# Optimization experiments

Hardware: AMD Instinct MI355X
Metric: run time of the kernel (lower is better)

## Reference

```python
import jax, jax.numpy as jnp
import numpy as np

N, E, R, D = 50000, 800000, 8, 64
BN_EPS = 1e-5


def _bn_relu(x, g, b):
    # training-mode BatchNorm1d (biased variance) + relu
    m = x.mean(axis=0)
    v = x.var(axis=0)
    return jax.nn.relu((x - m) / jnp.sqrt(v + BN_EPS) * g + b)


def setup_inputs() -> dict:
    key = jax.random.key(0)
    ks = jax.random.split(key, 10)
    return {
        'x': jax.random.normal(ks[0], (N, D), dtype=jnp.float32),
        'edge_weight': jax.random.uniform(ks[1], (E,), dtype=jnp.float32),
        'W_lin1': jax.random.normal(ks[2], (D, R * D), dtype=jnp.float32) * 0.05,
        'b_lin1': jnp.zeros((D,), jnp.float32),
        'W_self1': jax.random.normal(ks[3], (D, D), dtype=jnp.float32) * 0.05,
        'b_self1': jnp.zeros((D,), jnp.float32),
        'gamma1': jnp.ones((D,), jnp.float32),
        'beta1': jnp.zeros((D,), jnp.float32),
        'W_lin2': jax.random.normal(ks[4], (D, D), dtype=jnp.float32) * 0.05,
        'b_lin2': jnp.zeros((D,), jnp.float32),
        'W_self2': jax.random.normal(ks[5], (D, D), dtype=jnp.float32) * 0.05,
        'b_self2': jnp.zeros((D,), jnp.float32),
        'gamma2': jnp.ones((D,), jnp.float32),
        'beta2': jnp.zeros((D,), jnp.float32),
        'node_in': jax.random.randint(ks[6], (E,), 0, N, dtype=jnp.int32),
        'node_out': jax.random.randint(ks[7], (E,), 0, N, dtype=jnp.int32),
        'relation': jax.random.randint(ks[8], (E,), 0, R, dtype=jnp.int32),
        'num_relation': R,
    }


def reference(x, edge_weight, W_lin1, b_lin1, W_self1, b_self1, gamma1, beta1,
              W_lin2, b_lin2, W_self2, b_self2, gamma2, beta2,
              node_in, node_out, relation, num_relation):
    Nn, Din = x.shape
    Rr = int(num_relation)
    seg = node_out * Rr + relation  # node_out * num_relation + relation
    # degree normalization of edge weights (shared by both layers)
    deg = jax.ops.segment_sum(edge_weight, seg, num_segments=Nn * Rr)
    ew = edge_weight / deg[seg]

    # layer 1: relationalGraphConv
    msgs = x[node_in] * ew[:, None]  # [E, D]
    upd = jax.ops.segment_sum(msgs, seg, num_segments=Nn * Rr)
    upd = upd.reshape(Nn, Rr * Din)  # node-major flatten, matches torch .view
    h = upd @ W_lin1.T + b_lin1 + x @ W_self1.T + b_self1
    h = _bn_relu(h, gamma1, beta1)  # [N, D]

    # layer 2: relationalGraph (per-relation outputs)
    msgs2 = h[node_in] * ew[:, None]
    upd2 = jax.ops.segment_sum(msgs2, seg, num_segments=Nn * Rr)  # [N*R, D] node-major
    upd2 = upd2.reshape(Nn, Rr, -1).transpose(1, 0, 2).reshape(Rr * Nn, -1)  # relation-major
    h_rep = jnp.tile(h, (Rr, 1))  # input.repeat(R, 1)
    out = upd2 @ W_lin2.T + b_lin2 + h_rep @ W_self2.T + b_self2
    out = _bn_relu(out, gamma2, beta2)
    return out.reshape(Rr, Nn, -1)
```

## Files before the change

kernel.cpp:

```cpp
#include <hip/hip_runtime.h>


#define GATHER_GRID 2048
#define SCAN_CHUNK 4096
#define RED_BLOCKS 64
#define ZERO_BLOCKS 256
#define PACK_BLOCKS 16
#define XB_BLOCKS 64
#define COUNT_BLOCKS 2048
#define PLACE_BLOCKS 1024
#define STAT1_BLOCKS 512

typedef short bf16x8 __attribute__((ext_vector_type(8)));
typedef float f32x4 __attribute__((ext_vector_type(4)));

static __device__ __forceinline__ float bf2f(unsigned short u) {
  return __uint_as_float(((unsigned)u) << 16);
}
static __device__ __forceinline__ unsigned short f2bf(float f) {
  unsigned u = __float_as_uint(f);
  u += 0x7FFFu + ((u >> 16) & 1u);
  return (unsigned short)(u >> 16);
}

__global__ void k_zeropack(int* __restrict__ cnt, int NR, int R,
                           const float* __restrict__ Wlin1, const float* __restrict__ Wself1,
                           const float* __restrict__ Wlin2, const float* __restrict__ Wself2,
                           unsigned short* __restrict__ wb1, unsigned short* __restrict__ wb2) {
  if (blockIdx.x < ZERO_BLOCKS) {
    int i = blockIdx.x * 256 + threadIdx.x;
    int stride = ZERO_BLOCKS * 256;
    for (int k = i; k < NR; k += stride) cnt[k] = 0;
  } else {
    int i = (blockIdx.x - ZERO_BLOCKS) * 256 + threadIdx.x;
    int stride = PACK_BLOCKS * 256;
    int KW = R * 64 + 64;
    int n1 = 64 * KW;
    int n2 = 2 * 64 * 64;
    for (int t = i; t < n1 + n2; t += stride) {
      if (t < n1) {
        int j = t / KW, k = t - j * KW;
        float v = (k < R * 64) ? Wlin1[j * (R * 64) + k] : Wself1[j * 64 + (k - R * 64)];
        wb1[t] = f2bf(v);
      } else {
        int t2 = t - n1;
        int r = t2 >> 6, d = t2 & 63;
        float v = (r < 64) ? Wlin2[r * 64 + d] : Wself2[(r - 64) * 64 + d];
        wb2[t2] = f2bf(v);
      }
    }
  }
}

__global__ void k_countx(const int* __restrict__ node_out, const int* __restrict__ rel,
                         int* __restrict__ cnt, int* __restrict__ tmp, int E, int R,
                         const float4* __restrict__ xin, ushort4* __restrict__ xb, int n4) {
  if (blockIdx.x < XB_BLOCKS) {
    int i = blockIdx.x * 256 + threadIdx.x;
    int stride = XB_BLOCKS * 256;
    for (int k = i; k < n4; k += stride) {
      float4 v = xin[k];
      ushort4 o;
      o.x = f2bf(v.x); o.y = f2bf(v.y); o.z = f2bf(v.z); o.w = f2bf(v.w);
      xb[k] = o;
    }
  } else {
    int i = (blockIdx.x - XB_BLOCKS) * 256 + threadIdx.x;
    int stride = COUNT_BLOCKS * 256;
    for (int e = i; e < E; e += stride) {
      int seg = node_out[e] * R + rel[e];
      tmp[e] = atomicAdd(&cnt[seg], 1);
    }
  }
}

__global__ __launch_bounds__(256) void k_scan1(const int* __restrict__ cnt,
                                               int* __restrict__ bsum, int NR) {
  __shared__ int red[256];
  int tid = threadIdx.x;
  int base = blockIdx.x * SCAN_CHUNK;
  int s = 0;
  for (int i = tid; i < SCAN_CHUNK; i += 256) {
    int idx = base + i;
    if (idx < NR) s += cnt[idx];
  }
  red[tid] = s;
  __syncthreads();
  for (int off = 128; off > 0; off >>= 1) {
    if (tid < off) red[tid] += red[tid + off];
    __syncthreads();
  }
  if (tid == 0) bsum[blockIdx.x] = red[0];
}

__global__ void k_scan2(const int* __restrict__ bsum, int* __restrict__ bpre,
                        int* __restrict__ rowptr_end, int NB) {
  int lane = threadIdx.x;
  int carry = 0;
  for (int base = 0; base < NB; base += 64) {
    int i = base + lane;
    int v = (i < NB) ? bsum[i] : 0;
    int incl = v;
    #pragma unroll
    for (int off = 1; off < 64; off <<= 1) {
      int u = __shfl_up(incl, off);
      if (lane >= off) incl += u;
    }
    if (i < NB) bpre[i] = carry + incl - v;
    carry += __shfl(incl, 63);
  }
  if (lane == 0) *rowptr_end = carry;
}

__global__ __launch_bounds__(256) void k_scan3(const int* __restrict__ cnt,
                                               const int* __restrict__ bpre,
                                               int* __restrict__ rowptr, int NR) {
  __shared__ int wtot[4];
  int tid = threadIdx.x, lane = tid & 63, wid = tid >> 6;
  int base = blockIdx.x * SCAN_CHUNK + tid * 16;
  int v[16];
  int t = 0;
  #pragma unroll
  for (int i = 0; i < 16; i++) {
    int idx = base + i;
    v[i] = (idx < NR) ? cnt[idx] : 0;
    t += v[i];
  }
  int incl = t;
  #pragma unroll
  for (int off = 1; off < 64; off <<= 1) {
    int u = __shfl_up(incl, off);
    if (lane >= off) incl += u;
  }
  if (lane == 63) wtot[wid] = incl;
  __syncthreads();
  int woff = 0;
  for (int w = 0; w < wid; w++) woff += wtot[w];
  int start = bpre[blockIdx.x] + woff + incl - t;
  #pragma unroll
  for (int i = 0; i < 16; i++) {
    int idx = base + i;
    if (idx < NR) rowptr[idx] = start;
    start += v[i];
  }
}

__global__ void k_place(const float* __restrict__ w, const int* __restrict__ node_out,
                        const int* __restrict__ node_in, const int* __restrict__ rel,
                        const int* __restrict__ rowptr, const int* __restrict__ tmp,
                        unsigned* __restrict__ ep4, int E, int R) {
  int i = blockIdx.x * blockDim.x + threadIdx.x;
  int stride = gridDim.x * blockDim.x;
  for (int e = i; e < E; e += stride) {
    int seg = node_out[e] * R + rel[e];
    int pos = rowptr[seg] + tmp[e];
    ep4[pos] = (unsigned)node_in[e] | ((unsigned)f2bf(w[e]) << 16);
  }
}

__global__ void k_norm(const int* __restrict__ rowptr, unsigned* __restrict__ ep4, int NR) {
  int s = blockIdx.x * blockDim.x + threadIdx.x;
  if (s >= NR) return;
  int k0 = rowptr[s], k1 = rowptr[s + 1];
  if (k0 >= k1) return;
  float d = 0.f;
  for (int k = k0; k < k1; k++) d += bf2f((unsigned short)(ep4[k] >> 16));
  float inv = 1.f / d;
  for (int k = k0; k < k1; k++) {
    unsigned v = ep4[k];
    float w = bf2f((unsigned short)(v >> 16)) * inv;
    ep4[k] = (v & 0xFFFFu) | ((unsigned)f2bf(w) << 16);
  }
}

__global__ __launch_bounds__(256) void k_gatherx(
    const int* __restrict__ rowptr, const unsigned* __restrict__ ep4,
    const unsigned short* __restrict__ xb, unsigned short* __restrict__ updx,
    int N, int R) {
  int lane = threadIdx.x & 63;
  int wid = threadIdx.x >> 6;
  int l16 = lane & 15;
  int lg = lane >> 4;
  int c0 = l16 * 4;
  int grp = blockIdx.x * 16 + wid * 4 + lg;
  int ngrp = gridDim.x * 16;
  for (int n = grp; n < N; n += ngrp) {
    int segbase = n * R;
    int k = rowptr[segbase];
    for (int r = 0; r < R; r++) {
      int k1 = rowptr[segbase + r + 1];
      float a0 = 0.f, a1 = 0.f, a2 = 0.f, a3 = 0.f;
      for (; k + 1 < k1; k += 2) {
        unsigned pA = ep4[k], pB = ep4[k + 1];
        ushort4 uA = *(const ushort4*)&xb[(size_t)(pA & 0xFFFFu) * 64 + c0];
        ushort4 uB = *(const ushort4*)&xb[(size_t)(pB & 0xFFFFu) * 64 + c0];
        float wA = bf2f((unsigned short)(pA >> 16));
        float wB = bf2f((unsigned short)(pB >> 16));
        a0 = fmaf(wA, bf2f(uA.x), a0); a1 = fmaf(wA, bf2f(uA.y), a1);
        a2 = fmaf(wA, bf2f(uA.z), a2); a3 = fmaf(wA, bf2f(uA.w), a3);
        a0 = fmaf(wB, bf2f(uB.x), a0); a1 = fmaf(wB, bf2f(uB.y), a1);
        a2 = fmaf(wB, bf2f(uB.z), a2); a3 = fmaf(wB, bf2f(uB.w), a3);
      }
      if (k < k1) {
        unsigned p = ep4[k];
        float w = bf2f((unsigned short)(p >> 16));
        ushort4 u = *(const ushort4*)&xb[(size_t)(p & 0xFFFFu) * 64 + c0];
        a0 = fmaf(w, bf2f(u.x), a0); a1 = fmaf(w, bf2f(u.y), a1);
        a2 = fmaf(w, bf2f(u.z), a2); a3 = fmaf(w, bf2f(u.w), a3);
        k = k1;
      }
      ushort4 o; o.x = f2bf(a0); o.y = f2bf(a1); o.z = f2bf(a2); o.w = f2bf(a3);
      *(ushort4*)&updx[(size_t)n * 512 + r * 64 + c0] = o;
    }
  }
}

__global__ __launch_bounds__(256) void k_gemm1b(
    const unsigned short* __restrict__ updx, const unsigned short* __restrict__ xb,
    int M, const unsigned short* __restrict__ wb1, unsigned short* __restrict__ h_pre) {
  int m0 = blockIdx.x * 64;
  int wid = threadIdx.x >> 6;
  int lane = threadIdx.x & 63;
  int mrow = m0 + wid * 16 + (lane & 15);
  int mload = (mrow < M) ? mrow : (M - 1);
  int koff = 8 * (lane >> 4);
  const unsigned short* aU = updx + (size_t)mload * 512 + koff;
  const unsigned short* aX = xb + (size_t)mload * 64 + koff;
  const unsigned short* wr = wb1 + (size_t)(lane & 15) * 576 + koff;
  f32x4 acc[4] = {{0,0,0,0},{0,0,0,0},{0,0,0,0},{0,0,0,0}};
  #pragma unroll
  for (int kk = 0; kk < 16; ++kk) {
    bf16x8 a = *(const bf16x8*)(aU + kk * 32);
    #pragma unroll
    for (int nt = 0; nt < 4; ++nt) {
      bf16x8 b = *(const bf16x8*)(wr + (size_t)nt * 16 * 576 + kk * 32);
      acc[nt] = __builtin_amdgcn_mfma_f32_16x16x32_bf16(a, b, acc[nt], 0, 0, 0);
    }
  }
  #pragma unroll
  for (int kk = 0; kk < 2; ++kk) {
    bf16x8 a = *(const bf16x8*)(aX + kk * 32);
    #pragma unroll
    for (int nt = 0; nt < 4; ++nt) {
      bf16x8 b = *(const bf16x8*)(wr + (size_t)nt * 16 * 576 + 512 + kk * 32);
      acc[nt] = __builtin_amdgcn_mfma_f32_16x16x32_bf16(a, b, acc[nt], 0, 0, 0);
    }
  }
  int rbase = m0 + wid * 16 + ((lane >> 4) << 2);
  int cbase = lane & 15;
  #pragma unroll
  for (int nt = 0; nt < 4; ++nt) {
    int col = nt * 16 + cbase;
    #pragma unroll
    for (int rg = 0; rg < 4; ++rg) {
      int grow = rbase + rg;
      if (grow < M) h_pre[(size_t)grow * 64 + col] = f2bf(acc[nt][rg]);
    }
  }
}

__global__ __launch_bounds__(256) void k_stats1(const unsigned short* __restrict__ h,
                                                int N, float* __restrict__ part) {
  int j = threadIdx.x & 63;
  int rg = threadIdx.x >> 6;
  float s = 0.f, q = 0.f;
  for (int row = blockIdx.x * 4 + rg; row < N; row += gridDim.x * 4) {
    float v = bf2f(h[(size_t)row * 64 + j]);
    s += v; q += v * v;
  }
  __shared__ float sp[4][64], sq[4][64];
  sp[rg][j] = s; sq[rg][j] = q;
  __syncthreads();
  if (threadIdx.x < 64) {
    float ss = 0.f, qq = 0.f;
    for (int g = 0; g < 4; g++) { ss += sp[g][threadIdx.x]; qq += sq[g][threadIdx.x]; }
    part[(size_t)blockIdx.x * 128 + threadIdx.x] = ss;
    part[(size_t)blockIdx.x * 128 + 64 + threadIdx.x] = qq;
  }
}

__global__ __launch_bounds__(256) void k_gemm2bn(
    const unsigned short* __restrict__ hp, int M,
    const unsigned short* __restrict__ Wb, int nslab,
    const float* __restrict__ ss,
    unsigned short* __restrict__ outLinB, unsigned short* __restrict__ outSelf) {
  __shared__ float sss[128];
  if (threadIdx.x < 128) sss[threadIdx.x] = ss[threadIdx.x];
  __syncthreads();
  int m0 = blockIdx.x * 64;
  int wid = threadIdx.x >> 6;
  int lane = threadIdx.x & 63;
  int mrow = m0 + wid * 16 + (lane & 15);
  int mload = (mrow < M) ? mrow : (M - 1);
  int cb = 8 * (lane >> 4);
  const unsigned short* arow = hp + (size_t)mload * 64 + cb;
  ushort4 u0 = *(const ushort4*)(arow);
  ushort4 u1 = *(const ushort4*)(arow + 4);
  ushort4 u2 = *(const ushort4*)(arow + 32);
  ushort4 u3 = *(const ushort4*)(arow + 36);
  bf16x8 a0, a1;
  #pragma unroll
  for (int j = 0; j < 4; j++) {
    unsigned short uu0 = (&u0.x)[j], uu1 = (&u1.x)[j], uu2 = (&u2.x)[j], uu3 = (&u3.x)[j];
    a0[j]     = (short)f2bf(fmaxf(fmaf(bf2f(uu0), sss[cb + j],      sss[64 + cb + j]), 0.f));
    a0[j + 4] = (short)f2bf(fmaxf(fmaf(bf2f(uu1), sss[cb + 4 + j],  sss[64 + cb + 4 + j]), 0.f));
    a1[j]     = (short)f2bf(fmaxf(fmaf(bf2f(uu2), sss[cb + 32 + j], sss[64 + cb + 32 + j]), 0.f));
    a1[j + 4] = (short)f2bf(fmaxf(fmaf(bf2f(uu3), sss[cb + 36 + j], sss[64 + cb + 36 + j]), 0.f));
  }
  int rbase = m0 + wid * 16 + ((lane >> 4) << 2);
  int cbase = lane & 15;
  for (int slab = 0; slab <= nslab; ++slab) {
    const unsigned short* wrow = Wb + ((size_t)slab * 64 + (lane & 15)) * 64 + 8 * (lane >> 4);
    unsigned short* op = (slab < nslab) ? (outLinB + (size_t)slab * M * 64) : outSelf;
    #pragma unroll
    for (int nt = 0; nt < 4; ++nt) {
      bf16x8 b0 = *(const bf16x8*)(wrow + nt * 16 * 64);
      bf16x8 b1 = *(const bf16x8*)(wrow + nt * 16 * 64 + 32);
      f32x4 c = {};
      c = __builtin_amdgcn_mfma_f32_16x16x32_bf16(a0, b0, c, 0, 0, 0);
      c = __builtin_amdgcn_mfma_f32_16x16x32_bf16(a1, b1, c, 0, 0, 0);
      int col = nt * 16 + cbase;
      #pragma unroll
      for (int rg = 0; rg < 4; ++rg) {
        int grow = rbase + rg;
        if (grow < M) op[(size_t)grow * 64 + col] = f2bf(c[rg]);
      }
    }
  }
}

__global__ __launch_bounds__(256) void k_gather2_stats(
    const int* __restrict__ rowptr, const unsigned* __restrict__ ep4,
    const unsigned short* __restrict__ z, const unsigned short* __restrict__ s2,
    float* __restrict__ part, int N, int R) {
  int lane = threadIdx.x & 63;
  int wid = threadIdx.x >> 6;
  int l16 = lane & 15;
  int lg = lane >> 4;
  int c0 = l16 * 4;
  int grp = blockIdx.x * 16 + wid * 4 + lg;
  int ngrp = gridDim.x * 16;
  int NR = N * R;
  float lsum[4] = {0.f, 0.f, 0.f, 0.f}, lsq[4] = {0.f, 0.f, 0.f, 0.f};
  for (int s = grp; s < NR; s += ngrp) {
    unsigned r = (unsigned)s / (unsigned)N;
    int n = s - (int)r * N;
    int seg = n * R + (int)r;
    int k = rowptr[seg];
    int k1 = rowptr[seg + 1];
    float a0 = 0.f, a1 = 0.f, a2 = 0.f, a3 = 0.f;
    for (; k + 1 < k1; k += 2) {
      unsigned pA = ep4[k], pB = ep4[k + 1];
      ushort4 uA = *(const ushort4*)&z[(size_t)(pA & 0xFFFFu) * 64 + c0];
      ushort4 uB = *(const ushort4*)&z[(size_t)(pB & 0xFFFFu) * 64 + c0];
      float wA = bf2f((unsigned short)(pA >> 16));
      float wB = bf2f((unsigned short)(pB >> 16));
      a0 = fmaf(wA, bf2f(uA.x), a0); a1 = fmaf(wA, bf2f(uA.y), a1);
      a2 = fmaf(wA, bf2f(uA.z), a2); a3 = fmaf(wA, bf2f(uA.w), a3);
      a0 = fmaf(wB, bf2f(uB.x), a0); a1 = fmaf(wB, bf2f(uB.y), a1);
      a2 = fmaf(wB, bf2f(uB.z), a2); a3 = fmaf(wB, bf2f(uB.w), a3);
    }
    if (k < k1) {
      unsigned p = ep4[k];
      float w = bf2f((unsigned short)(p >> 16));
      ushort4 u = *(const ushort4*)&z[(size_t)(p & 0xFFFFu) * 64 + c0];
      a0 = fmaf(w, bf2f(u.x), a0); a1 = fmaf(w, bf2f(u.y), a1);
      a2 = fmaf(w, bf2f(u.z), a2); a3 = fmaf(w, bf2f(u.w), a3);
    }
    ushort4 su = *(const ushort4*)&s2[(size_t)n * 64 + c0];
    float v0 = a0 + bf2f(su.x), v1 = a1 + bf2f(su.y);
    float v2 = a2 + bf2f(su.z), v3 = a3 + bf2f(su.w);
    lsum[0] += v0; lsq[0] += v0 * v0;
    lsum[1] += v1; lsq[1] += v1 * v1;
    lsum[2] += v2; lsq[2] += v2 * v2;
    lsum[3] += v3; lsq[3] += v3 * v3;
  }
  __shared__ float sp[16][64], sq[16][64];
  int g = wid * 4 + lg;
  #pragma unroll
  for (int i = 0; i < 4; i++) { sp[g][c0 + i] = lsum[i]; sq[g][c0 + i] = lsq[i]; }
  __syncthreads();
  if (threadIdx.x < 64) {
    int j = threadIdx.x;
    float s = 0.f, q = 0.f;
    #pragma unroll
    for (int gg = 0; gg < 16; gg++) { s += sp[gg][j]; q += sq[gg][j]; }
    part[(size_t)blockIdx.x * 128 + j] = s;
    part[(size_t)blockIdx.x * 128 + 64 + j] = q;
  }
}

__global__ __launch_bounds__(256) void k_gather2_write(
    const int* __restrict__ rowptr, const unsigned* __restrict__ ep4,
    const unsigned short* __restrict__ z, const unsigned short* __restrict__ s2,
    const float* __restrict__ ss, float* __restrict__ out, int N, int R) {
  int lane = threadIdx.x & 63;
  int wid = threadIdx.x >> 6;
  int l16 = lane & 15;
  int lg = lane >> 4;
  int c0 = l16 * 4;
  float sc0 = ss[c0], sc1 = ss[c0 + 1], sc2 = ss[c0 + 2], sc3 = ss[c0 + 3];
  float sh0 = ss[64 + c0], sh1 = ss[64 + c0 + 1], sh2 = ss[64 + c0 + 2], sh3 = ss[64 + c0 + 3];
  int grp = blockIdx.x * 16 + wid * 4 + lg;
  int ngrp = gridDim.x * 16;
  int NR = N * R;
  for (int s = grp; s < NR; s += ngrp) {
    unsigned r = (unsigned)s / (unsigned)N;
    int n = s - (int)r * N;
    int seg = n * R + (int)r;
    int k = rowptr[seg];
    int k1 = rowptr[seg + 1];
    float a0 = 0.f, a1 = 0.f, a2 = 0.f, a3 = 0.f;
    for (; k + 1 < k1; k += 2) {
      unsigned pA = ep4[k], pB = ep4[k + 1];
      ushort4 uA = *(const ushort4*)&z[(size_t)(pA & 0xFFFFu) * 64 + c0];
      ushort4 uB = *(const ushort4*)&z[(size_t)(pB & 0xFFFFu) * 64 + c0];
      float wA = bf2f((unsigned short)(pA >> 16));
      float wB = bf2f((unsigned short)(pB >> 16));
      a0 = fmaf(wA, bf2f(uA.x), a0); a1 = fmaf(wA, bf2f(uA.y), a1);
      a2 = fmaf(wA, bf2f(uA.z), a2); a3 = fmaf(wA, bf2f(uA.w), a3);
      a0 = fmaf(wB, bf2f(uB.x), a0); a1 = fmaf(wB, bf2f(uB.y), a1);
      a2 = fmaf(wB, bf2f(uB.z), a2); a3 = fmaf(wB, bf2f(uB.w), a3);
    }
    if (k < k1) {
      unsigned p = ep4[k];
      float w = bf2f((unsigned short)(p >> 16));
      ushort4 u = *(const ushort4*)&z[(size_t)(p & 0xFFFFu) * 64 + c0];
      a0 = fmaf(w, bf2f(u.x), a0); a1 = fmaf(w, bf2f(u.y), a1);
      a2 = fmaf(w, bf2f(u.z), a2); a3 = fmaf(w, bf2f(u.w), a3);
    }
    ushort4 su = *(const ushort4*)&s2[(size_t)n * 64 + c0];
    float v0 = fmaxf(fmaf(a0 + bf2f(su.x), sc0, sh0), 0.f);
    float v1 = fmaxf(fmaf(a1 + bf2f(su.y), sc1, sh1), 0.f);
    float v2 = fmaxf(fmaf(a2 + bf2f(su.z), sc2, sh2), 0.f);
    float v3 = fmaxf(fmaf(a3 + bf2f(su.w), sc3, sh3), 0.f);
    *(float4*)&out[(size_t)s * 64 + c0] = make_float4(v0, v1, v2, v3);
  }
}

__global__ __launch_bounds__(256) void k_red1(const float* __restrict__ part,
                                              float* __restrict__ part2, int P) {
  int j = threadIdx.x & 127;
  int g = threadIdx.x >> 7;
  int rows = (P + RED_BLOCKS - 1) / RED_BLOCKS;
  int base = blockIdx.x * rows;
  float acc = 0.f;
  for (int i = g; i < rows; i += 2) {
    int idx = base + i;
    if (idx < P) acc += part[(size_t)idx * 128 + j];
  }
  __shared__ float red[2][128];
  red[g][j] = acc;
  __syncthreads();
  if (threadIdx.x < 128) part2[(size_t)blockIdx.x * 128 + j] = red[0][j] + red[1][j];
}

__global__ __launch_bounds__(1024) void k_bnstats(
    const float* __restrict__ part, int P, float M,
    const float* __restrict__ gamma, const float* __restrict__ beta,
    float* __restrict__ ss) {
  __shared__ float red[1024];
  int tid = threadIdx.x;
  int j = tid & 127;
  int g = tid >> 7;
  float acc = 0.f;
  for (int i = g; i < P; i += 8) acc += part[(size_t)i * 128 + j];
  red[tid] = acc;
  __syncthreads();
  if (tid < 128) {
    float s = 0.f;
    for (int gg = 0; gg < 8; gg++) s += red[gg * 128 + tid];
    red[tid] = s;
  }
  __syncthreads();
  if (tid < 64) {
    float s = red[tid], q = red[64 + tid];
    float mean = s / M;
    float var = q / M - mean * mean;
    float sc = gamma[tid] / sqrtf(var + 1e-5f);
    ss[tid] = sc;
    ss[64 + tid] = beta[tid] - mean * sc;
  }
}

extern "C" void kernel_launch(void* const* d_in, const int* in_sizes, int n_in,
                              void* d_out, int out_size, void* d_ws, size_t ws_size,
                              hipStream_t stream) {
  const float* x        = (const float*)d_in[0];
  const float* edge_w   = (const float*)d_in[1];
  const float* W_lin1   = (const float*)d_in[2];
  const float* W_self1  = (const float*)d_in[4];
  const float* gamma1   = (const float*)d_in[6];
  const float* beta1    = (const float*)d_in[7];
  const float* W_lin2   = (const float*)d_in[8];
  const float* W_self2  = (const float*)d_in[10];
  const float* gamma2   = (const float*)d_in[12];
  const float* beta2    = (const float*)d_in[13];
  const int* node_in    = (const int*)d_in[14];
  const int* node_out   = (const int*)d_in[15];
  const int* relation   = (const int*)d_in[16];

  int N = in_sizes[0] / 64;
  int E = in_sizes[1];
  int R = in_sizes[2] / (64 * 64);
  int NR = N * R;
  int NB = (NR + SCAN_CHUNK - 1) / SCAN_CHUNK;

  char* p = (char*)d_ws;
  auto alloc = [&](size_t bytes) { char* r = p; p += (bytes + 255) & ~(size_t)255; return r; };
  int* cnt      = (int*)alloc(4ull * NR);
  int* rowptr   = (int*)alloc(4ull * (NR + 1));
  int* tmp      = (int*)alloc(4ull * E);
  int* bsum     = (int*)alloc(4ull * NB);
  int* bpre     = (int*)alloc(4ull * NB);
  unsigned* ep4 = (unsigned*)alloc(4ull * E);
  unsigned short* wb1 = (unsigned short*)alloc(2ull * 64 * (R * 64 + 64));
  unsigned short* wb2 = (unsigned short*)alloc(2ull * 2 * 64 * 64);
  unsigned short* h_pre = (unsigned short*)alloc(2ull * N * 64);
  unsigned short* z     = (unsigned short*)alloc(2ull * N * 64);
  unsigned short* s2    = (unsigned short*)alloc(2ull * N * 64);
  float* part   = (float*)alloc(4ull * GATHER_GRID * 128);
  float* part2  = (float*)alloc(4ull * RED_BLOCKS * 128);
  float* ss1    = (float*)alloc(4ull * 128);
  float* ss2    = (float*)alloc(4ull * 128);

  unsigned short* updx = (unsigned short*)d_out;
  unsigned short* xb   = updx + (size_t)N * 512;

  int mblocks = (N + 63) / 64;

  k_zeropack<<<ZERO_BLOCKS + PACK_BLOCKS, 256, 0, stream>>>(
      cnt, NR, R, W_lin1, W_self1, W_lin2, W_self2, wb1, wb2);
  k_countx<<<XB_BLOCKS + COUNT_BLOCKS, 256, 0, stream>>>(
      node_out, relation, cnt, tmp, E, R, (const float4*)x, (ushort4*)xb, N * 64 / 4);
  k_scan1<<<NB, 256, 0, stream>>>(cnt, bsum, NR);
  k_scan2<<<1, 64, 0, stream>>>(bsum, bpre, &rowptr[NR], NB);
  k_scan3<<<NB, 256, 0, stream>>>(cnt, bpre, rowptr, NR);
  k_place<<<PLACE_BLOCKS, 256, 0, stream>>>(
      edge_w, node_out, node_in, relation, rowptr, tmp, ep4, E, R);
  k_norm<<<(NR + 255) / 256, 256, 0, stream>>>(rowptr, ep4, NR);

  k_gatherx<<<GATHER_GRID, 256, 0, stream>>>(rowptr, ep4, xb, updx, N, R);
  k_gemm1b<<<mblocks, 256, 0, stream>>>(updx, xb, N, wb1, h_pre);
  k_stats1<<<STAT1_BLOCKS, 256, 0, stream>>>(h_pre, N, part);
  k_red1<<<RED_BLOCKS, 256, 0, stream>>>(part, part2, STAT1_BLOCKS);
  k_bnstats<<<1, 1024, 0, stream>>>(part2, RED_BLOCKS, (float)N, gamma1, beta1, ss1);

  k_gemm2bn<<<mblocks, 256, 0, stream>>>(h_pre, N, wb2, 1, ss1, z, s2);
  k_gather2_stats<<<GATHER_GRID, 256, 0, stream>>>(rowptr, ep4, z, s2, part, N, R);
  k_red1<<<RED_BLOCKS, 256, 0, stream>>>(part, part2, GATHER_GRID);
  k_bnstats<<<1, 1024, 0, stream>>>(part2, RED_BLOCKS, (float)N * R, gamma2, beta2, ss2);
  k_gather2_write<<<GATHER_GRID, 256, 0, stream>>>(rowptr, ep4, z, s2, ss2, (float*)d_out, N, R);
}
```

Before: 284.4 us.

## Fuse layer-1 gather, GEMM and BN stats; fold degree normalization into gathers

Layer 1's gather of neighbour features now writes into a shared-memory tile that the MFMA GEMM reads directly, and the BN statistics are computed from the accumulators in the same kernel. This removes the round trip of the large updx buffer through global memory and drops the separate stats kernel. The separate k_norm pass is removed: each gather accumulates the weight sum and divides by it in registers. The scan also writes a relation-major descriptor table (start and count packed into one word) so the layer-2 gathers read one contiguous word per segment instead of two scattered rowptr entries. The packing limits edge offsets to 20 bits and per-segment counts to 12 bits, and the fused kernel launches more blocks with extra synchronisation.

```diff
diff --git a/kernel.cpp b/kernel.cpp
--- a/kernel.cpp
+++ b/kernel.cpp
@@ -9,7 +9,7 @@
 #define XB_BLOCKS 64
 #define COUNT_BLOCKS 2048
 #define PLACE_BLOCKS 1024
-#define STAT1_BLOCKS 512
+#define L1_NODES 32
 
 typedef short bf16x8 __attribute__((ext_vector_type(8)));
 typedef float f32x4 __attribute__((ext_vector_type(4)));
@@ -114,7 +114,9 @@
 
 __global__ __launch_bounds__(256) void k_scan3(const int* __restrict__ cnt,
                                                const int* __restrict__ bpre,
-                                               int* __restrict__ rowptr, int NR) {
+                                               int* __restrict__ rowptr,
+                                               unsigned* __restrict__ descT,
+                                               int NR, int R, int Nn) {
   __shared__ int wtot[4];
   int tid = threadIdx.x, lane = tid & 63, wid = tid >> 6;
   int base = blockIdx.x * SCAN_CHUNK + tid * 16;
@@ -140,7 +142,12 @@
   #pragma unroll
   for (int i = 0; i < 16; i++) {
     int idx = base + i;
-    if (idx < NR) rowptr[idx] = start;
+    if (idx < NR) {
+      rowptr[idx] = start;
+      int n = (int)((unsigned)idx / (unsigned)R);
+      int r = idx - n * R;
+      descT[(size_t)r * Nn + n] = (unsigned)start | ((unsigned)v[i] << 20);
+    }
     start += v[i];
   }
 }
@@ -158,124 +165,118 @@
   }
 }
 
-__global__ void k_norm(const int* __restrict__ rowptr, unsigned* __restrict__ ep4, int NR) {
-  int s = blockIdx.x * blockDim.x + threadIdx.x;
-  if (s >= NR) return;
-  int k0 = rowptr[s], k1 = rowptr[s + 1];
-  if (k0 >= k1) return;
-  float d = 0.f;
-  for (int k = k0; k < k1; k++) d += bf2f((unsigned short)(ep4[k] >> 16));
-  float inv = 1.f / d;
-  for (int k = k0; k < k1; k++) {
-    unsigned v = ep4[k];
-    float w = bf2f((unsigned short)(v >> 16)) * inv;
-    ep4[k] = (v & 0xFFFFu) | ((unsigned)f2bf(w) << 16);
-  }
-}
-
-__global__ __launch_bounds__(256) void k_gatherx(
+__global__ __launch_bounds__(256) void k_layer1(
     const int* __restrict__ rowptr, const unsigned* __restrict__ ep4,
-    const unsigned short* __restrict__ xb, unsigned short* __restrict__ updx,
-    int N, int R) {
-  int lane = threadIdx.x & 63;
-  int wid = threadIdx.x >> 6;
-  int l16 = lane & 15;
-  int lg = lane >> 4;
-  int c0 = l16 * 4;
-  int grp = blockIdx.x * 16 + wid * 4 + lg;
-  int ngrp = gridDim.x * 16;
-  for (int n = grp; n < N; n += ngrp) {
-    int segbase = n * R;
-    int k = rowptr[segbase];
-    for (int r = 0; r < R; r++) {
-      int k1 = rowptr[segbase + r + 1];
-      float a0 = 0.f, a1 = 0.f, a2 = 0.f, a3 = 0.f;
-      for (; k + 1 < k1; k += 2) {
-        unsigned pA = ep4[k], pB = ep4[k + 1];
-        ushort4 uA = *(const ushort4*)&xb[(size_t)(pA & 0xFFFFu) * 64 + c0];
-        ushort4 uB = *(const ushort4*)&xb[(size_t)(pB & 0xFFFFu) * 64 + c0];
-        float wA = bf2f((unsigned short)(pA >> 16));
-        float wB = bf2f((unsigned short)(pB >> 16));
-        a0 = fmaf(wA, bf2f(uA.x), a0); a1 = fmaf(wA, bf2f(uA.y), a1);
-        a2 = fmaf(wA, bf2f(uA.z), a2); a3 = fmaf(wA, bf2f(uA.w), a3);
-        a0 = fmaf(wB, bf2f(uB.x), a0); a1 = fmaf(wB, bf2f(uB.y), a1);
-        a2 = fmaf(wB, bf2f(uB.z), a2); a3 = fmaf(wB, bf2f(uB.w), a3);
-      }
-      if (k < k1) {
-        unsigned p = ep4[k];
-        float w = bf2f((unsigned short)(p >> 16));
-        ushort4 u = *(const ushort4*)&xb[(size_t)(p & 0xFFFFu) * 64 + c0];
-        a0 = fmaf(w, bf2f(u.x), a0); a1 = fmaf(w, bf2f(u.y), a1);
-        a2 = fmaf(w, bf2f(u.z), a2); a3 = fmaf(w, bf2f(u.w), a3);
-        k = k1;
+    const unsigned short* __restrict__ xb, const unsigned short* __restrict__ wb1,
+    unsigned short* __restrict__ h_pre, float* __restrict__ part, int M, int R) {
+  __shared__ unsigned short tile[L1_NODES][520];
+  int tid = threadIdx.x;
+  int n0 = blockIdx.x * L1_NODES;
+  {
+    int gid = tid >> 4;
+    int l16 = tid & 15;
+    int c0 = l16 * 4;
+    int nseg = L1_NODES * R;
+    for (int sl = gid; sl < nseg; sl += 16) {
+      int nl = (int)((unsigned)sl / (unsigned)R);
+      int r = sl - nl * R;
+      int n = n0 + nl;
+      float a0 = 0.f, a1 = 0.f, a2 = 0.f, a3 = 0.f, d = 0.f;
+      if (n < M) {
+        int seg = n * R + r;
+        int k = rowptr[seg], k1 = rowptr[seg + 1];
+        for (; k + 1 < k1; k += 2) {
+          unsigned pA = ep4[k], pB = ep4[k + 1];
+          ushort4 uA = *(const ushort4*)&xb[(size_t)(pA & 0xFFFFu) * 64 + c0];
+          ushort4 uB = *(const ushort4*)&xb[(size_t)(pB & 0xFFFFu) * 64 + c0];
+          float wA = bf2f((unsigned short)(pA >> 16));
+          float wB = bf2f((unsigned short)(pB >> 16));
+          d += wA + wB;
+          a0 = fmaf(wA, bf2f(uA.x), a0); a1 = fmaf(wA, bf2f(uA.y), a1);
+          a2 = fmaf(wA, bf2f(uA.z), a2); a3 = fmaf(wA, bf2f(uA.w), a3);
+          a0 = fmaf(wB, bf2f(uB.x), a0); a1 = fmaf(wB, bf2f(uB.y), a1);
+          a2 = fmaf(wB, bf2f(uB.z), a2); a3 = fmaf(wB, bf2f(uB.w), a3);
+        }
+        if (k < k1) {
+          unsigned p = ep4[k];
+          float w = bf2f((unsigned short)(p >> 16));
+          ushort4 u = *(const ushort4*)&xb[(size_t)(p & 0xFFFFu) * 64 + c0];
+          d += w;
+          a0 = fmaf(w, bf2f(u.x), a0); a1 = fmaf(w, bf2f(u.y), a1);
+          a2 = fmaf(w, bf2f(u.z), a2); a3 = fmaf(w, bf2f(u.w), a3);
+        }
+        if (d != 0.f) {
+          float inv = 1.f / d;
+          a0 *= inv; a1 *= inv; a2 *= inv; a3 *= inv;
+        }
       }
       ushort4 o; o.x = f2bf(a0); o.y = f2bf(a1); o.z = f2bf(a2); o.w = f2bf(a3);
-      *(ushort4*)&updx[(size_t)n * 512 + r * 64 + c0] = o;
-    }
-  }
-}
-
-__global__ __launch_bounds__(256) void k_gemm1b(
-    const unsigned short* __restrict__ updx, const unsigned short* __restrict__ xb,
-    int M, const unsigned short* __restrict__ wb1, unsigned short* __restrict__ h_pre) {
-  int m0 = blockIdx.x * 64;
-  int wid = threadIdx.x >> 6;
-  int lane = threadIdx.x & 63;
-  int mrow = m0 + wid * 16 + (lane & 15);
-  int mload = (mrow < M) ? mrow : (M - 1);
+      *(ushort4*)&tile[nl][r * 64 + c0] = o;
+    }
+  }
+  __syncthreads();
+  int w = tid >> 6, lane = tid & 63;
+  int rloc = (w & 1) * 16 + (lane & 15);
   int koff = 8 * (lane >> 4);
-  const unsigned short* aU = updx + (size_t)mload * 512 + koff;
-  const unsigned short* aX = xb + (size_t)mload * 64 + koff;
+  const unsigned short* arow = &tile[rloc][koff];
+  int gxrow = n0 + rloc; if (gxrow >= M) gxrow = M - 1;
+  const unsigned short* aX = xb + (size_t)gxrow * 64 + koff;
+  int ntbase = (w >> 1) * 2;
   const unsigned short* wr = wb1 + (size_t)(lane & 15) * 576 + koff;
-  f32x4 acc[4] = {{0,0,0,0},{0,0,0,0},{0,0,0,0},{0,0,0,0}};
+  f32x4 acc[2] = {{0, 0, 0, 0}, {0, 0, 0, 0}};
   #pragma unroll
   for (int kk = 0; kk < 16; ++kk) {
-    bf16x8 a = *(const bf16x8*)(aU + kk * 32);
-    #pragma unroll
-    for (int nt = 0; nt < 4; ++nt) {
-      bf16x8 b = *(const bf16x8*)(wr + (size_t)nt * 16 * 576 + kk * 32);
-      acc[nt] = __builtin_amdgcn_mfma_f32_16x16x32_bf16(a, b, acc[nt], 0, 0, 0);
+    bf16x8 a = *(const bf16x8*)(arow + kk * 32);
+    #pragma unroll
+    for (int t = 0; t < 2; ++t) {
+      bf16x8 b = *(const bf16x8*)(wr + (size_t)(ntbase + t) * 16 * 576 + kk * 32);
+      acc[t] = __builtin_amdgcn_mfma_f32_16x16x32_bf16(a, b, acc[t], 0, 0, 0);
     }
   }
   #pragma unroll
   for (int kk = 0; kk < 2; ++kk) {
     bf16x8 a = *(const bf16x8*)(aX + kk * 32);
     #pragma unroll
-    for (int nt = 0; nt < 4; ++nt) {
-      bf16x8 b = *(const bf16x8*)(wr + (size_t)nt * 16 * 576 + 512 + kk * 32);
-      acc[nt] = __builtin_amdgcn_mfma_f32_16x16x32_bf16(a, b, acc[nt], 0, 0, 0);
-    }
-  }
-  int rbase = m0 + wid * 16 + ((lane >> 4) << 2);
+    for (int t = 0; t < 2; ++t) {
+      bf16x8 b = *(const bf16x8*)(wr + (size_t)(ntbase + t) * 16 * 576 + 512 + kk * 32);
+      acc[t] = __builtin_amdgcn_mfma_f32_16x16x32_bf16(a, b, acc[t], 0, 0, 0);
+    }
+  }
   int cbase = lane & 15;
-  #pragma unroll
-  for (int nt = 0; nt < 4; ++nt) {
-    int col = nt * 16 + cbase;
+  int rbase_loc = (w & 1) * 16 + ((lane >> 4) << 2);
+  #pragma unroll
+  for (int t = 0; t < 2; ++t) {
+    int col = (ntbase + t) * 16 + cbase;
     #pragma unroll
     for (int rg = 0; rg < 4; ++rg) {
-      int grow = rbase + rg;
-      if (grow < M) h_pre[(size_t)grow * 64 + col] = f2bf(acc[nt][rg]);
-    }
-  }
-}
-
-__global__ __launch_bounds__(256) void k_stats1(const unsigned short* __restrict__ h,
-                                                int N, float* __restrict__ part) {
-  int j = threadIdx.x & 63;
-  int rg = threadIdx.x >> 6;
-  float s = 0.f, q = 0.f;
-  for (int row = blockIdx.x * 4 + rg; row < N; row += gridDim.x * 4) {
-    float v = bf2f(h[(size_t)row * 64 + j]);
-    s += v; q += v * v;
-  }
-  __shared__ float sp[4][64], sq[4][64];
-  sp[rg][j] = s; sq[rg][j] = q;
-  __syncthreads();
-  if (threadIdx.x < 64) {
-    float ss = 0.f, qq = 0.f;
-    for (int g = 0; g < 4; g++) { ss += sp[g][threadIdx.x]; qq += sq[g][threadIdx.x]; }
-    part[(size_t)blockIdx.x * 128 + threadIdx.x] = ss;
-    part[(size_t)blockIdx.x * 128 + 64 + threadIdx.x] = qq;
+      int grow = n0 + rbase_loc + rg;
+      if (grow < M) h_pre[(size_t)grow * 64 + col] = f2bf(acc[t][rg]);
+    }
+  }
+  __syncthreads();
+  float* sp = (float*)&tile[0][0];
+  float* sq = sp + 8 * 64;
+  int strip = (w & 1) * 4 + (lane >> 4);
+  #pragma unroll
+  for (int t = 0; t < 2; ++t) {
+    float cs = 0.f, cq = 0.f;
+    #pragma unroll
+    for (int rg = 0; rg < 4; ++rg) {
+      int grow = n0 + rbase_loc + rg;
+      float v = (grow < M) ? acc[t][rg] : 0.f;
+      cs += v; cq += v * v;
+    }
+    int col = (ntbase + t) * 16 + cbase;
+    sp[strip * 64 + col] = cs;
+    sq[strip * 64 + col] = cq;
+  }
+  __syncthreads();
+  if (tid < 64) {
+    float s = 0.f, q = 0.f;
+    #pragma unroll
+    for (int g = 0; g < 8; g++) { s += sp[g * 64 + tid]; q += sq[g * 64 + tid]; }
+    part[(size_t)blockIdx.x * 128 + tid] = s;
+    part[(size_t)blockIdx.x * 128 + 64 + tid] = q;
   }
 }
 
@@ -330,7 +331,7 @@
 }
 
 __global__ __launch_bounds__(256) void k_gather2_stats(
-    const int* __restrict__ rowptr, const unsigned* __restrict__ ep4,
+    const unsigned* __restrict__ descT, const unsigned* __restrict__ ep4,
     const unsigned short* __restrict__ z, const unsigned short* __restrict__ s2,
     float* __restrict__ part, int N, int R) {
   int lane = threadIdx.x & 63;
@@ -345,16 +346,18 @@
   for (int s = grp; s < NR; s += ngrp) {
     unsigned r = (unsigned)s / (unsigned)N;
     int n = s - (int)r * N;
-    int seg = n * R + (int)r;
-    int k = rowptr[seg];
-    int k1 = rowptr[seg + 1];
-    float a0 = 0.f, a1 = 0.f, a2 = 0.f, a3 = 0.f;
+    unsigned desc = descT[s];
+    int k = (int)(desc & 0xFFFFFu);
+    int cnt = (int)(desc >> 20);
+    int k1 = k + cnt;
+    float a0 = 0.f, a1 = 0.f, a2 = 0.f, a3 = 0.f, d = 0.f;
     for (; k + 1 < k1; k += 2) {
       unsigned pA = ep4[k], pB = ep4[k + 1];
       ushort4 uA = *(const ushort4*)&z[(size_t)(pA & 0xFFFFu) * 64 + c0];
       ushort4 uB = *(const ushort4*)&z[(size_t)(pB & 0xFFFFu) * 64 + c0];
       float wA = bf2f((unsigned short)(pA >> 16));
       float wB = bf2f((unsigned short)(pB >> 16));
+      d += wA + wB;
       a0 = fmaf(wA, bf2f(uA.x), a0); a1 = fmaf(wA, bf2f(uA.y), a1);
       a2 = fmaf(wA, bf2f(uA.z), a2); a3 = fmaf(wA, bf2f(uA.w), a3);
       a0 = fmaf(wB, bf2f(uB.x), a0); a1 = fmaf(wB, bf2f(uB.y), a1);
@@ -364,8 +367,13 @@
       unsigned p = ep4[k];
       float w = bf2f((unsigned short)(p >> 16));
       ushort4 u = *(const ushort4*)&z[(size_t)(p & 0xFFFFu) * 64 + c0];
+      d += w;
       a0 = fmaf(w, bf2f(u.x), a0); a1 = fmaf(w, bf2f(u.y), a1);
       a2 = fmaf(w, bf2f(u.z), a2); a3 = fmaf(w, bf2f(u.w), a3);
+    }
+    if (d != 0.f) {
+      float inv = 1.f / d;
+      a0 *= inv; a1 *= inv; a2 *= inv; a3 *= inv;
     }
     ushort4 su = *(const ushort4*)&s2[(size_t)n * 64 + c0];
     float v0 = a0 + bf2f(su.x), v1 = a1 + bf2f(su.y);
@@ -391,7 +399,7 @@
 }
 
 __global__ __launch_bounds__(256) void k_gather2_write(
-    const int* __restrict__ rowptr, const unsigned* __restrict__ ep4,
+    const unsigned* __restrict__ descT, const unsigned* __restrict__ ep4,
     const unsigned short* __restrict__ z, const unsigned short* __restrict__ s2,
     const float* __restrict__ ss, float* __restrict__ out, int N, int R) {
   int lane = threadIdx.x & 63;
@@ -407,16 +415,18 @@
   for (int s = grp; s < NR; s += ngrp) {
     unsigned r = (unsigned)s / (unsigned)N;
     int n = s - (int)r * N;
-    int seg = n * R + (int)r;
-    int k = rowptr[seg];
-    int k1 = rowptr[seg + 1];
-    float a0 = 0.f, a1 = 0.f, a2 = 0.f, a3 = 0.f;
+    unsigned desc = descT[s];
+    int k = (int)(desc & 0xFFFFFu);
+    int cnt = (int)(desc >> 20);
+    int k1 = k + cnt;
+    float a0 = 0.f, a1 = 0.f, a2 = 0.f, a3 = 0.f, d = 0.f;
     for (; k + 1 < k1; k += 2) {
       unsigned pA = ep4[k], pB = ep4[k + 1];
       ushort4 uA = *(const ushort4*)&z[(size_t)(pA & 0xFFFFu) * 64 + c0];
       ushort4 uB = *(const ushort4*)&z[(size_t)(pB & 0xFFFFu) * 64 + c0];
       float wA = bf2f((unsigned short)(pA >> 16));
       float wB = bf2f((unsigned short)(pB >> 16));
+      d += wA + wB;
       a0 = fmaf(wA, bf2f(uA.x), a0); a1 = fmaf(wA, bf2f(uA.y), a1);
       a2 = fmaf(wA, bf2f(uA.z), a2); a3 = fmaf(wA, bf2f(uA.w), a3);
       a0 = fmaf(wB, bf2f(uB.x), a0); a1 = fmaf(wB, bf2f(uB.y), a1);
@@ -426,8 +436,13 @@
       unsigned p = ep4[k];
       float w = bf2f((unsigned short)(p >> 16));
       ushort4 u = *(const ushort4*)&z[(size_t)(p & 0xFFFFu) * 64 + c0];
+      d += w;
       a0 = fmaf(w, bf2f(u.x), a0); a1 = fmaf(w, bf2f(u.y), a1);
       a2 = fmaf(w, bf2f(u.z), a2); a3 = fmaf(w, bf2f(u.w), a3);
+    }
+    if (d != 0.f) {
+      float inv = 1.f / d;
+      a0 *= inv; a1 *= inv; a2 *= inv; a3 *= inv;
     }
     ushort4 su = *(const ushort4*)&s2[(size_t)n * 64 + c0];
     float v0 = fmaxf(fmaf(a0 + bf2f(su.x), sc0, sh0), 0.f);
@@ -510,12 +525,14 @@
   auto alloc = [&](size_t bytes) { char* r = p; p += (bytes + 255) & ~(size_t)255; return r; };
   int* cnt      = (int*)alloc(4ull * NR);
   int* rowptr   = (int*)alloc(4ull * (NR + 1));
+  unsigned* descT = (unsigned*)alloc(4ull * NR);
   int* tmp      = (int*)alloc(4ull * E);
   int* bsum     = (int*)alloc(4ull * NB);
   int* bpre     = (int*)alloc(4ull * NB);
   unsigned* ep4 = (unsigned*)alloc(4ull * E);
   unsigned short* wb1 = (unsigned short*)alloc(2ull * 64 * (R * 64 + 64));
   unsigned short* wb2 = (unsigned short*)alloc(2ull * 2 * 64 * 64);
+  unsigned short* xb    = (unsigned short*)alloc(2ull * N * 64);
   unsigned short* h_pre = (unsigned short*)alloc(2ull * N * 64);
   unsigned short* z     = (unsigned short*)alloc(2ull * N * 64);
   unsigned short* s2    = (unsigned short*)alloc(2ull * N * 64);
@@ -524,10 +541,8 @@
   float* ss1    = (float*)alloc(4ull * 128);
   float* ss2    = (float*)alloc(4ull * 128);
 
-  unsigned short* updx = (unsigned short*)d_out;
-  unsigned short* xb   = updx + (size_t)N * 512;
-
-  int mblocks = (N + 63) / 64;
+  int mblocks1 = (N + L1_NODES - 1) / L1_NODES;
+  int mblocks  = (N + 63) / 64;
 
   k_zeropack<<<ZERO_BLOCKS + PACK_BLOCKS, 256, 0, stream>>>(
       cnt, NR, R, W_lin1, W_self1, W_lin2, W_self2, wb1, wb2);
@@ -535,20 +550,17 @@
       node_out, relation, cnt, tmp, E, R, (const float4*)x, (ushort4*)xb, N * 64 / 4);
   k_scan1<<<NB, 256, 0, stream>>>(cnt, bsum, NR);
   k_scan2<<<1, 64, 0, stream>>>(bsum, bpre, &rowptr[NR], NB);
-  k_scan3<<<NB, 256, 0, stream>>>(cnt, bpre, rowptr, NR);
+  k_scan3<<<NB, 256, 0, stream>>>(cnt, bpre, rowptr, descT, NR, R, N);
   k_place<<<PLACE_BLOCKS, 256, 0, stream>>>(
       edge_w, node_out, node_in, relation, rowptr, tmp, ep4, E, R);
-  k_norm<<<(NR + 255) / 256, 256, 0, stream>>>(rowptr, ep4, NR);
-
-  k_gatherx<<<GATHER_GRID, 256, 0, stream>>>(rowptr, ep4, xb, updx, N, R);
-  k_gemm1b<<<mblocks, 256, 0, stream>>>(updx, xb, N, wb1, h_pre);
-  k_stats1<<<STAT1_BLOCKS, 256, 0, stream>>>(h_pre, N, part);
-  k_red1<<<RED_BLOCKS, 256, 0, stream>>>(part, part2, STAT1_BLOCKS);
+
+  k_layer1<<<mblocks1, 256, 0, stream>>>(rowptr, ep4, xb, wb1, h_pre, part, N, R);
+  k_red1<<<RED_BLOCKS, 256, 0, stream>>>(part, part2, mblocks1);
   k_bnstats<<<1, 1024, 0, stream>>>(part2, RED_BLOCKS, (float)N, gamma1, beta1, ss1);
 
   k_gemm2bn<<<mblocks, 256, 0, stream>>>(h_pre, N, wb2, 1, ss1, z, s2);
-  k_gather2_stats<<<GATHER_GRID, 256, 0, stream>>>(rowptr, ep4, z, s2, part, N, R);
+  k_gather2_stats<<<GATHER_GRID, 256, 0, stream>>>(descT, ep4, z, s2, part, N, R);
   k_red1<<<RED_BLOCKS, 256, 0, stream>>>(part, part2, GATHER_GRID);
   k_bnstats<<<1, 1024, 0, stream>>>(part2, RED_BLOCKS, (float)N * R, gamma2, beta2, ss2);
-  k_gather2_write<<<GATHER_GRID, 256, 0, stream>>>(rowptr, ep4, z, s2, ss2, (float*)d_out, N, R);
-}
+  k_gather2_write<<<GATHER_GRID, 256, 0, stream>>>(descT, ep4, z, s2, ss2, (float*)d_out, N, R);
+}
```

Result: no change. 285.3 us (median of 2 runs) (+0.3%).
